# Optimization experiments

Hardware: AMD Instinct MI355X
Metric: run time of the kernel (lower is better)

Reference implementation:

```python
import jax, jax.numpy as jnp
import numpy as np

N = 131072       # active sparse sites (fixed)
C_IN = 256       # FPN input channels
HID = 512        # CONV_HEAD_DIM
K = 9            # 3x3 kernel taps
LAYERS = 8       # NUM_STACKED_CONVS
GROUPS = 32      # GroupNorm groups (detectron2 default)
EPS = 1e-5


def _build_rulebook(rng):
    # Sample sparse occupancy over 64 ROIs of 64x64, build 3x3 neighbor map.
    B, H, W = 64, 64, 64
    mask = rng.random((B, H, W)) < 0.60
    coords = np.argwhere(mask)[:N]          # [N,3] (b,y,x), fixed N
    assert coords.shape[0] == N
    grid = -np.ones((B, H + 2, W + 2), np.int32)  # padded, -1 = inactive
    grid[coords[:, 0], coords[:, 1] + 1, coords[:, 2] + 1] = np.arange(N, dtype=np.int32)
    offs = [(dy, dx) for dy in (-1, 0, 1) for dx in (-1, 0, 1)]
    nbr = np.stack(
        [grid[coords[:, 0], coords[:, 1] + 1 + dy, coords[:, 2] + 1 + dx] for dy, dx in offs],
        axis=1,
    )  # [N,9], -1 where neighbor inactive (submanifold: output sites == input sites)
    return nbr


def setup_inputs() -> dict:
    rng = np.random.default_rng(0)
    nbr = _build_rulebook(rng)
    key = jax.random.key(0)
    k0, k1, k2, k3, k4 = jax.random.split(key, 5)
    features = jax.random.normal(k0, (N, C_IN), jnp.float32)
    w0 = jax.random.normal(k1, (K, C_IN, HID), jnp.float32) * (1.0 / np.sqrt(K * C_IN))
    w_rest = jax.random.normal(k2, (LAYERS - 1, K, HID, HID), jnp.float32) * (1.0 / np.sqrt(K * HID))
    gamma = 1.0 + 0.1 * jax.random.normal(k3, (LAYERS, HID), jnp.float32)
    beta = 0.1 * jax.random.normal(k4, (LAYERS, HID), jnp.float32)
    return {
        "features": features,
        "nbr_idx": jnp.asarray(nbr),
        "w0": w0,
        "w_rest": w_rest,
        "gamma": gamma,
        "beta": beta,
    }


def _subm_conv(x, nbr_idx, w):
    # gather-GEMM-scatter submanifold conv: x [N,Cin], nbr_idx [N,K], w [K,Cin,Cout]
    n = x.shape[0]
    xp = jnp.concatenate([x, jnp.zeros((1, x.shape[1]), x.dtype)], axis=0)  # zero row for -1
    idx = jnp.where(nbr_idx < 0, n, nbr_idx)
    out = jnp.zeros((n, w.shape[2]), x.dtype)
    for k in range(K):  # fixed small loop over kernel taps
        out = out + xp[idx[:, k]] @ w[k]
    return out


def _group_norm(x, g, b):
    # per-point GroupNorm over channel groups: x [N,C]
    n, c = x.shape
    xg = x.reshape(n, GROUPS, c // GROUPS)
    mu = jnp.mean(xg, axis=-1, keepdims=True)
    var = jnp.var(xg, axis=-1, keepdims=True)
    xg = (xg - mu) * jax.lax.rsqrt(var + EPS)
    return xg.reshape(n, c) * g + b


def reference(features, nbr_idx, w0, w_rest, gamma, beta):
    x = jax.nn.relu(_group_norm(_subm_conv(features, nbr_idx, w0), gamma[0], beta[0]))
    for i in range(LAYERS - 1):
        x = jax.nn.relu(_group_norm(_subm_conv(x, nbr_idx, w_rest[i]), gamma[i + 1], beta[i + 1]))
    return x
```

## Files before the change

### kernel.cpp

```cpp
#include <hip/hip_runtime.h>
#include <stdint.h>

#define N_SITES 131072
#define CIN0 256
#define HID 512
#define KTAPS 9
#define NLAYERS 8

typedef __bf16 bf16x8 __attribute__((ext_vector_type(8)));
typedef float f32x4 __attribute__((ext_vector_type(4)));

__device__ __forceinline__ unsigned short f2bf(float f) {
    union { float f; unsigned u; } v; v.f = f;
    return (unsigned short)((v.u + 0x7fffu + ((v.u >> 16) & 1u)) >> 16);
}


__global__ void cvt_features_kernel(const float* __restrict__ in, unsigned short* __restrict__ out) {
    int t = blockIdx.x * 256 + threadIdx.x;
    const float4* p = (const float4*)in + 2 * (size_t)t;
    float4 a = p[0], b = p[1];
    uint4 o;
    o.x = f2bf(a.x) | ((unsigned)f2bf(a.y) << 16);
    o.y = f2bf(a.z) | ((unsigned)f2bf(a.w) << 16);
    o.z = f2bf(b.x) | ((unsigned)f2bf(b.y) << 16);
    o.w = f2bf(b.z) | ((unsigned)f2bf(b.w) << 16);
    ((uint4*)out)[t] = o;
}

__global__ void zero_rows_kernel(unsigned short* __restrict__ xf, unsigned short* __restrict__ xo) {
    int t = threadIdx.x;
    xf[(size_t)N_SITES * 512 + t] = 0;
    xf[(size_t)N_SITES * 512 + 256 + t] = 0;
    xo[(size_t)N_SITES * 256 + t] = 0;
    xo[(size_t)N_SITES * 512 + t] = 0;
    xo[(size_t)N_SITES * 512 + 256 + t] = 0;
}

__global__ void transpose_w_kernel(const float* __restrict__ in, unsigned short* __restrict__ out, int cin) {
    __shared__ float tile[32][33];
    int m = blockIdx.z;
    int nb = blockIdx.x * 32;
    int cb = blockIdx.y * 32;
    int tx = threadIdx.x, ty = threadIdx.y;
    const float* src = in + (size_t)m * cin * HID;
    unsigned short* dst = out + (size_t)m * HID * cin;
#pragma unroll
    for (int j = 0; j < 4; ++j) {
        int r = ty + 8 * j;
        tile[r][tx] = src[(size_t)(cb + r) * HID + nb + tx];
    }
    __syncthreads();
#pragma unroll
    for (int j = 0; j < 4; ++j) {
        int r = ty + 8 * j;
        dst[(size_t)(nb + r) * cin + cb + tx] = f2bf(tile[tx][r]);
    }
}


__device__ __forceinline__ void async16(const void* g, void* l) {
    __builtin_amdgcn_global_load_lds(
        (__attribute__((address_space(1))) unsigned int*)(g),
        (__attribute__((address_space(3))) unsigned int*)(l),
        16, 0, 0);
}

#define BARRIER() do { asm volatile("" ::: "memory"); __builtin_amdgcn_s_barrier(); asm volatile("" ::: "memory"); } while (0)
#define WAIT_LGKM0() asm volatile("s_waitcnt lgkmcnt(0)" ::: "memory")
#define WAIT_VM4() asm volatile("s_waitcnt vmcnt(4)" ::: "memory")
#define WAIT_VM0() asm volatile("s_waitcnt vmcnt(0)" ::: "memory")

#define MFMA4(I, A, B0_, B1_, B2_, B3_) \
    acc[I][0] = __builtin_amdgcn_mfma_f32_16x16x32_bf16(A, B0_, acc[I][0], 0, 0, 0); \
    acc[I][1] = __builtin_amdgcn_mfma_f32_16x16x32_bf16(A, B1_, acc[I][1], 0, 0, 0); \
    acc[I][2] = __builtin_amdgcn_mfma_f32_16x16x32_bf16(A, B2_, acc[I][2], 0, 0, 0); \
    acc[I][3] = __builtin_amdgcn_mfma_f32_16x16x32_bf16(A, B3_, acc[I][3], 0, 0, 0);

template<int CIN>
__global__ __launch_bounds__(512, 2) void subm_gemm_gn_8ph(
    const unsigned short* __restrict__ x,
    const int* __restrict__ nbr,
    const unsigned short* __restrict__ wt,
    const float* __restrict__ gamma,
    const float* __restrict__ beta,
    void* __restrict__ obuf,
    int write_bf16)
{
    constexpr int KK = CIN / 64;
    __shared__ uint4 lds[8192];
    __shared__ int nbrS[256 * KTAPS];

    const int tid = threadIdx.x;
    const int lane = tid & 63;
    const int wave = tid >> 6;
    const int wm = (wave >> 2) * 128;
    const int wn = (wave & 3) * 64;

    const int b = (int)blockIdx.x;
    const int xcd = b & 7;
    const int slot = b >> 3;
    const int colbase = (xcd & 1) * 256;
    const int rowbase = ((xcd >> 1) * 128 + slot) * 256;

    const int srow = 2 * (tid >> 3) + ((tid >> 2) & 1);
    const int scl = (tid & 3) ^ ((tid >> 3) & 3);
    const int ldsw = tid & ~63;

    for (int u = tid; u < 256 * KTAPS; u += 512) {
        int v = nbr[(size_t)rowbase * KTAPS + u];
        nbrS[u] = (v < 0) ? N_SITES : v;
    }
    __syncthreads();

    const f32x4 zero4 = {0.f, 0.f, 0.f, 0.f};
    f32x4 acc[8][4];
#pragma unroll
    for (int i = 0; i < 8; ++i)
#pragma unroll
        for (int j = 0; j < 4; ++j)
            acc[i][j] = zero4;

    auto stageA = [&](int i0, int i1, int kkp, int kh, int buf) {
        const unsigned short* g0 = x + (size_t)i0 * CIN + kkp * 64 + kh * 32 + scl * 8;
        const unsigned short* g1 = x + (size_t)i1 * CIN + kkp * 64 + kh * 32 + scl * 8;
        async16(g0, &lds[buf * 4096 + kh * 1024 + ldsw]);
        async16(g1, &lds[buf * 4096 + kh * 1024 + 512 + ldsw]);
    };
    auto stageB = [&](int tp, int kkp, int kh, int buf) {
        const unsigned short* g0 = wt + (size_t)(tp * HID + colbase + srow) * CIN + kkp * 64 + kh * 32 + scl * 8;
        const unsigned short* g1 = wt + (size_t)(tp * HID + colbase + srow + 128) * CIN + kkp * 64 + kh * 32 + scl * 8;
        async16(g0, &lds[buf * 4096 + 2048 + kh * 1024 + ldsw]);
        async16(g1, &lds[buf * 4096 + 2048 + kh * 1024 + 512 + ldsw]);
    };
    auto rdA = [&](int i, int ks, int buf) {
        int rl = wm + i * 16 + (lane & 15);
        return __builtin_bit_cast(bf16x8,
            lds[buf * 4096 + ks * 1024 + (rl >> 1) * 8 + (rl & 1) * 4 + ((lane >> 4) ^ ((rl >> 1) & 3))]);
    };
    auto rdB = [&](int j, int ks, int buf) {
        int rn = wn + j * 16 + (lane & 15);
        return __builtin_bit_cast(bf16x8,
            lds[buf * 4096 + 2048 + ks * 1024 + (rn >> 1) * 8 + (rn & 1) * 4 + ((lane >> 4) ^ ((rn >> 1) & 3))]);
    };

    {
        int a0 = nbrS[srow * KTAPS], a1 = nbrS[(srow + 128) * KTAPS];
        stageA(a0, a1, 0, 0, 0);
        stageB(0, 0, 0, 0);
        stageA(a0, a1, 0, 1, 0);
        stageB(0, 0, 1, 0);
    }
    WAIT_VM4();
    BARRIER();

    for (int tap = 0; tap < KTAPS; ++tap) {
#pragma unroll 2
        for (int kk = 0; kk < KK; ++kk) {
            const int p = kk & 1;
            const int q = p ^ 1;
            const bool haveNext = !(tap == KTAPS - 1 && kk == KK - 1);
            const int ntap = (kk == KK - 1) ? tap + 1 : tap;
            const int nkk = (kk == KK - 1) ? 0 : kk + 1;
            int nA0 = 0, nA1 = 0;
            if (haveNext) {
                nA0 = nbrS[srow * KTAPS + ntap];
                nA1 = nbrS[(srow + 128) * KTAPS + ntap];
            }
            if (haveNext) stageA(nA0, nA1, nkk, 0, q);
            bf16x8 a0 = rdA(0, 0, p), a1 = rdA(1, 0, p), a2 = rdA(2, 0, p), a3 = rdA(3, 0, p);
            bf16x8 b0 = rdB(0, 0, p), b1 = rdB(1, 0, p), b2 = rdB(2, 0, p), b3 = rdB(3, 0, p);
            BARRIER();
            WAIT_LGKM0();
            __builtin_amdgcn_s_setprio(1);
            MFMA4(0, a0, b0, b1, b2, b3)
            MFMA4(1, a1, b0, b1, b2, b3)
            MFMA4(2, a2, b0, b1, b2, b3)
            MFMA4(3, a3, b0, b1, b2, b3)
            __builtin_amdgcn_s_setprio(0);
            BARRIER();
            if (haveNext) stageB(ntap, nkk, 0, q);
            {
                bf16x8 a4 = rdA(4, 0, p), a5 = rdA(5, 0, p), a6 = rdA(6, 0, p), a7 = rdA(7, 0, p);
                BARRIER();
                WAIT_LGKM0();
                __builtin_amdgcn_s_setprio(1);
                MFMA4(4, a4, b0, b1, b2, b3)
                MFMA4(5, a5, b0, b1, b2, b3)
                MFMA4(6, a6, b0, b1, b2, b3)
                MFMA4(7, a7, b0, b1, b2, b3)
                __builtin_amdgcn_s_setprio(0);
            }
            if (haveNext) { WAIT_VM4(); } else { WAIT_VM0(); }
            BARRIER();
            if (haveNext) stageA(nA0, nA1, nkk, 1, q);
            a0 = rdA(0, 1, p); a1 = rdA(1, 1, p); a2 = rdA(2, 1, p); a3 = rdA(3, 1, p);
            b0 = rdB(0, 1, p); b1 = rdB(1, 1, p); b2 = rdB(2, 1, p); b3 = rdB(3, 1, p);
            BARRIER();
            WAIT_LGKM0();
            __builtin_amdgcn_s_setprio(1);
            MFMA4(0, a0, b0, b1, b2, b3)
            MFMA4(1, a1, b0, b1, b2, b3)
            MFMA4(2, a2, b0, b1, b2, b3)
            MFMA4(3, a3, b0, b1, b2, b3)
            __builtin_amdgcn_s_setprio(0);
            BARRIER();
            if (haveNext) stageB(ntap, nkk, 1, q);
            {
                bf16x8 a4 = rdA(4, 1, p), a5 = rdA(5, 1, p), a6 = rdA(6, 1, p), a7 = rdA(7, 1, p);
                BARRIER();
                WAIT_LGKM0();
                __builtin_amdgcn_s_setprio(1);
                MFMA4(4, a4, b0, b1, b2, b3)
                MFMA4(5, a5, b0, b1, b2, b3)
                MFMA4(6, a6, b0, b1, b2, b3)
                MFMA4(7, a7, b0, b1, b2, b3)
                __builtin_amdgcn_s_setprio(0);
            }
            WAIT_VM4();
            BARRIER();
        }
    }

    __syncthreads();
    float* E = (float*)lds;
    const int seg = tid & 31;
    const int qv = tid >> 5;
    const int c0s = seg * 8;
    unsigned short* bf_out = (unsigned short*)obuf;
    float* f_out = (float*)obuf;

    float gv[8], bv[8];
#pragma unroll
    for (int k = 0; k < 8; ++k) {
        gv[k] = gamma[colbase + c0s + k];
        bv[k] = beta[colbase + c0s + k];
    }

#pragma unroll
    for (int pass = 0; pass < 2; ++pass) {
        if (pass) __syncthreads();
#pragma unroll
        for (int ii = 0; ii < 4; ++ii) {
#pragma unroll
            for (int j = 0; j < 4; ++j) {
                const int col = wn + j * 16 + (lane & 15);
                const int lrow = (wm >> 1) + ii * 16 + (lane >> 4) * 4;
                *(f32x4*)&E[col * 128 + (lrow ^ (((col >> 3) & 7) << 2))] = acc[pass * 4 + ii][j];
            }
        }
        __syncthreads();
#pragma unroll
        for (int h = 0; h < 2; ++h) {
            const int r0w = (qv + h * 16) * 4;
            f32x4 vv[8];
            f32x4 s = zero4, q2 = zero4;
#pragma unroll
            for (int cc = 0; cc < 8; ++cc) {
                const int col = c0s + cc;
                vv[cc] = *(const f32x4*)&E[col * 128 + (r0w ^ (((col >> 3) & 7) << 2))];
                s += vv[cc];
                q2 += vv[cc] * vv[cc];
            }
            f32x4 mu, rs;
#pragma unroll
            for (int r = 0; r < 4; ++r) {
                s[r] += __shfl_xor(s[r], 1);
                q2[r] += __shfl_xor(q2[r], 1);
                mu[r] = s[r] * 0.0625f;
                rs[r] = rsqrtf(q2[r] * 0.0625f - mu[r] * mu[r] + 1e-5f);
            }
            if (write_bf16) {
#pragma unroll
                for (int r = 0; r < 4; ++r) {
                    const int l = r0w + r;
                    const int grow = rowbase + 64 * pass + (l & 63) + ((l >> 6) << 7);
                    unsigned pk[4];
#pragma unroll
                    for (int cp = 0; cp < 4; ++cp) {
                        float ya = fmaxf(0.f, (vv[2 * cp][r] - mu[r]) * rs[r] * gv[2 * cp] + bv[2 * cp]);
                        float yb = fmaxf(0.f, (vv[2 * cp + 1][r] - mu[r]) * rs[r] * gv[2 * cp + 1] + bv[2 * cp + 1]);
                        pk[cp] = f2bf(ya) | ((unsigned)f2bf(yb) << 16);
                    }
                    uint4 o; o.x = pk[0]; o.y = pk[1]; o.z = pk[2]; o.w = pk[3];
                    *(uint4*)&bf_out[(size_t)grow * HID + colbase + c0s] = o;
                }
            } else {
#pragma unroll
                for (int r = 0; r < 4; ++r) {
                    const int l = r0w + r;
                    const int grow = rowbase + 64 * pass + (l & 63) + ((l >> 6) << 7);
                    f32x4 ya, yb;
#pragma unroll
                    for (int k = 0; k < 4; ++k) {
                        ya[k] = fmaxf(0.f, (vv[k][r] - mu[r]) * rs[r] * gv[k] + bv[k]);
                        yb[k] = fmaxf(0.f, (vv[4 + k][r] - mu[r]) * rs[r] * gv[4 + k] + bv[4 + k]);
                    }
                    float* dst = f_out + (size_t)grow * HID + colbase + c0s;
                    *(f32x4*)dst = ya;
                    *(f32x4*)(dst + 4) = yb;
                }
            }
        }
    }
}


extern "C" void kernel_launch(void* const* d_in, const int* in_sizes, int n_in,
                              void* d_out, int out_size, void* d_ws, size_t ws_size,
                              hipStream_t stream) {
    const float* features = (const float*)d_in[0];
    const int*   nbr      = (const int*)d_in[1];
    const float* w0       = (const float*)d_in[2];
    const float* w_rest   = (const float*)d_in[3];
    const float* gamma    = (const float*)d_in[4];
    const float* beta     = (const float*)d_in[5];

    unsigned short* xF = (unsigned short*)d_ws;
    size_t xbytes = (size_t)(N_SITES + 1) * HID * sizeof(unsigned short);
    unsigned short* w0t = (unsigned short*)((char*)d_ws + xbytes);
    size_t w0t_bytes = (size_t)KTAPS * HID * CIN0 * sizeof(unsigned short);
    unsigned short* wrt = (unsigned short*)((char*)d_ws + xbytes + w0t_bytes);
    unsigned short* xO = (unsigned short*)d_out;

    cvt_features_kernel<<<N_SITES * CIN0 / (256 * 8), 256, 0, stream>>>(features, xO);
    zero_rows_kernel<<<1, 256, 0, stream>>>(xF, xO);
    transpose_w_kernel<<<dim3(HID / 32, CIN0 / 32, KTAPS), dim3(32, 8), 0, stream>>>(w0, w0t, CIN0);
    transpose_w_kernel<<<dim3(HID / 32, HID / 32, (NLAYERS - 1) * KTAPS), dim3(32, 8), 0, stream>>>(w_rest, wrt, HID);

    for (int l = 0; l < NLAYERS; ++l) {
        const unsigned short* wt = (l == 0) ? w0t : wrt + (size_t)(l - 1) * KTAPS * HID * HID;
        const unsigned short* xin = (l & 1) ? xF : xO;
        void* obuf = (l == NLAYERS - 1) ? d_out : (void*)((l & 1) ? xO : xF);
        const float* g = gamma + (size_t)l * HID;
        const float* bt = beta + (size_t)l * HID;
        int wb = (l < NLAYERS - 1) ? 1 : 0;
        if (l == 0)
            subm_gemm_gn_8ph<CIN0><<<(N_SITES / 256) * 2, 512, 0, stream>>>(xin, nbr, wt, g, bt, obuf, wb);
        else
            subm_gemm_gn_8ph<HID><<<(N_SITES / 256) * 2, 512, 0, stream>>>(xin, nbr, wt, g, bt, obuf, wb);
    }
}
```

Before: 5.352 ms.

## Shrink block tile to 128 rows with 3-stage single-barrier pipeline

Each block now covers 128 rows instead of 256 (grid doubles), with a 32-wide K step and a three-slot LDS ring buffer. Each iteration issues the loads for two steps ahead and ends with a single barrier, replacing the previous 8-phase schedule that used many barriers per step. LDS use and the accumulator count drop by half, and launch bounds target 4 blocks per CU to raise occupancy. The trade-off is that each weight tile is reused across fewer rows, so weight traffic doubles, and each MFMA burst between barriers is shorter.

```diff
diff --git a/kernel.cpp b/kernel.cpp
--- a/kernel.cpp
+++ b/kernel.cpp
@@ -67,18 +67,11 @@
 }
 
 #define BARRIER() do { asm volatile("" ::: "memory"); __builtin_amdgcn_s_barrier(); asm volatile("" ::: "memory"); } while (0)
-#define WAIT_LGKM0() asm volatile("s_waitcnt lgkmcnt(0)" ::: "memory")
-#define WAIT_VM4() asm volatile("s_waitcnt vmcnt(4)" ::: "memory")
+#define WAIT_VM3() asm volatile("s_waitcnt vmcnt(3)" ::: "memory")
 #define WAIT_VM0() asm volatile("s_waitcnt vmcnt(0)" ::: "memory")
 
-#define MFMA4(I, A, B0_, B1_, B2_, B3_) \
-    acc[I][0] = __builtin_amdgcn_mfma_f32_16x16x32_bf16(A, B0_, acc[I][0], 0, 0, 0); \
-    acc[I][1] = __builtin_amdgcn_mfma_f32_16x16x32_bf16(A, B1_, acc[I][1], 0, 0, 0); \
-    acc[I][2] = __builtin_amdgcn_mfma_f32_16x16x32_bf16(A, B2_, acc[I][2], 0, 0, 0); \
-    acc[I][3] = __builtin_amdgcn_mfma_f32_16x16x32_bf16(A, B3_, acc[I][3], 0, 0, 0);
-
 template<int CIN>
-__global__ __launch_bounds__(512, 2) void subm_gemm_gn_8ph(
+__global__ __launch_bounds__(512, 4) void subm_gemm_gn_p2(
     const unsigned short* __restrict__ x,
     const int* __restrict__ nbr,
     const unsigned short* __restrict__ wt,
@@ -87,139 +80,94 @@
     void* __restrict__ obuf,
     int write_bf16)
 {
-    constexpr int KK = CIN / 64;
-    __shared__ uint4 lds[8192];
-    __shared__ int nbrS[256 * KTAPS];
+    constexpr int KK = CIN / 32;
+    __shared__ uint4 lds[4608];
+    __shared__ int nbrS[128 * KTAPS];
 
     const int tid = threadIdx.x;
     const int lane = tid & 63;
     const int wave = tid >> 6;
-    const int wm = (wave >> 2) * 128;
+    const int wm = (wave >> 2) * 64;
     const int wn = (wave & 3) * 64;
 
     const int b = (int)blockIdx.x;
     const int xcd = b & 7;
     const int slot = b >> 3;
     const int colbase = (xcd & 1) * 256;
-    const int rowbase = ((xcd >> 1) * 128 + slot) * 256;
+    const int rowbase = ((xcd >> 1) * 256 + slot) * 128;
 
     const int srow = 2 * (tid >> 3) + ((tid >> 2) & 1);
     const int scl = (tid & 3) ^ ((tid >> 3) & 3);
     const int ldsw = tid & ~63;
 
-    for (int u = tid; u < 256 * KTAPS; u += 512) {
+    for (int u = tid; u < 128 * KTAPS; u += 512) {
         int v = nbr[(size_t)rowbase * KTAPS + u];
         nbrS[u] = (v < 0) ? N_SITES : v;
     }
     __syncthreads();
 
     const f32x4 zero4 = {0.f, 0.f, 0.f, 0.f};
-    f32x4 acc[8][4];
-#pragma unroll
-    for (int i = 0; i < 8; ++i)
+    f32x4 acc[4][4];
+#pragma unroll
+    for (int i = 0; i < 4; ++i)
 #pragma unroll
         for (int j = 0; j < 4; ++j)
             acc[i][j] = zero4;
 
-    auto stageA = [&](int i0, int i1, int kkp, int kh, int buf) {
-        const unsigned short* g0 = x + (size_t)i0 * CIN + kkp * 64 + kh * 32 + scl * 8;
-        const unsigned short* g1 = x + (size_t)i1 * CIN + kkp * 64 + kh * 32 + scl * 8;
-        async16(g0, &lds[buf * 4096 + kh * 1024 + ldsw]);
-        async16(g1, &lds[buf * 4096 + kh * 1024 + 512 + ldsw]);
-    };
-    auto stageB = [&](int tp, int kkp, int kh, int buf) {
-        const unsigned short* g0 = wt + (size_t)(tp * HID + colbase + srow) * CIN + kkp * 64 + kh * 32 + scl * 8;
-        const unsigned short* g1 = wt + (size_t)(tp * HID + colbase + srow + 128) * CIN + kkp * 64 + kh * 32 + scl * 8;
-        async16(g0, &lds[buf * 4096 + 2048 + kh * 1024 + ldsw]);
-        async16(g1, &lds[buf * 4096 + 2048 + kh * 1024 + 512 + ldsw]);
-    };
-    auto rdA = [&](int i, int ks, int buf) {
+    auto stageA = [&](int trow, int kk2, int s) {
+        async16(x + (size_t)trow * CIN + kk2 * 32 + scl * 8, &lds[s * 512 + ldsw]);
+    };
+    auto stageB = [&](int ttap, int kk2, int s) {
+        const unsigned short* g = wt + ((size_t)ttap * HID + colbase + srow) * CIN + kk2 * 32 + scl * 8;
+        async16(g, &lds[1536 + s * 1024 + ldsw]);
+        async16(g + (size_t)128 * CIN, &lds[1536 + s * 1024 + 512 + ldsw]);
+    };
+    auto rdA = [&](int i, int s) {
         int rl = wm + i * 16 + (lane & 15);
         return __builtin_bit_cast(bf16x8,
-            lds[buf * 4096 + ks * 1024 + (rl >> 1) * 8 + (rl & 1) * 4 + ((lane >> 4) ^ ((rl >> 1) & 3))]);
-    };
-    auto rdB = [&](int j, int ks, int buf) {
+            lds[s * 512 + (rl >> 1) * 8 + (rl & 1) * 4 + ((lane >> 4) ^ ((rl >> 1) & 3))]);
+    };
+    auto rdB = [&](int j, int s) {
         int rn = wn + j * 16 + (lane & 15);
         return __builtin_bit_cast(bf16x8,
-            lds[buf * 4096 + 2048 + ks * 1024 + (rn >> 1) * 8 + (rn & 1) * 4 + ((lane >> 4) ^ ((rn >> 1) & 3))]);
-    };
-
-    {
-        int a0 = nbrS[srow * KTAPS], a1 = nbrS[(srow + 128) * KTAPS];
-        stageA(a0, a1, 0, 0, 0);
-        stageB(0, 0, 0, 0);
-        stageA(a0, a1, 0, 1, 0);
-        stageB(0, 0, 1, 0);
-    }
-    WAIT_VM4();
+            lds[1536 + s * 1024 + (rn >> 1) * 8 + (rn & 1) * 4 + ((lane >> 4) ^ ((rn >> 1) & 3))]);
+    };
+
+    int rcur = nbrS[srow * KTAPS + 0];
+    stageA(rcur, 0, 0);
+    stageB(0, 0, 0);
+    stageA(rcur, 1, 1);
+    stageB(0, 1, 1);
+    WAIT_VM3();
     BARRIER();
 
+    int cur = 0;
     for (int tap = 0; tap < KTAPS; ++tap) {
-#pragma unroll 2
+        const int rnext = (tap + 1 < KTAPS) ? nbrS[srow * KTAPS + tap + 1] : 0;
         for (int kk = 0; kk < KK; ++kk) {
-            const int p = kk & 1;
-            const int q = p ^ 1;
-            const bool haveNext = !(tap == KTAPS - 1 && kk == KK - 1);
-            const int ntap = (kk == KK - 1) ? tap + 1 : tap;
-            const int nkk = (kk == KK - 1) ? 0 : kk + 1;
-            int nA0 = 0, nA1 = 0;
-            if (haveNext) {
-                nA0 = nbrS[srow * KTAPS + ntap];
-                nA1 = nbrS[(srow + 128) * KTAPS + ntap];
-            }
-            if (haveNext) stageA(nA0, nA1, nkk, 0, q);
-            bf16x8 a0 = rdA(0, 0, p), a1 = rdA(1, 0, p), a2 = rdA(2, 0, p), a3 = rdA(3, 0, p);
-            bf16x8 b0 = rdB(0, 0, p), b1 = rdB(1, 0, p), b2 = rdB(2, 0, p), b3 = rdB(3, 0, p);
+            const bool haveStage = !(tap == KTAPS - 1 && kk >= KK - 2);
+            const int stg = (cur >= 1) ? cur - 1 : 2;
+            if (haveStage) {
+                int kk2 = kk + 2, ttap = tap, trow = rcur;
+                if (kk2 >= KK) { kk2 -= KK; ttap = tap + 1; trow = rnext; }
+                stageA(trow, kk2, stg);
+                stageB(ttap, kk2, stg);
+            }
+            bf16x8 af[4], bfr[4];
+#pragma unroll
+            for (int f = 0; f < 4; ++f) { af[f] = rdA(f, cur); bfr[f] = rdB(f, cur); }
+            __builtin_amdgcn_s_setprio(1);
+#pragma unroll
+            for (int i = 0; i < 4; ++i)
+#pragma unroll
+                for (int j = 0; j < 4; ++j)
+                    acc[i][j] = __builtin_amdgcn_mfma_f32_16x16x32_bf16(af[i], bfr[j], acc[i][j], 0, 0, 0);
+            __builtin_amdgcn_s_setprio(0);
+            if (haveStage) { WAIT_VM3(); } else { WAIT_VM0(); }
             BARRIER();
-            WAIT_LGKM0();
-            __builtin_amdgcn_s_setprio(1);
-            MFMA4(0, a0, b0, b1, b2, b3)
-            MFMA4(1, a1, b0, b1, b2, b3)
-            MFMA4(2, a2, b0, b1, b2, b3)
-            MFMA4(3, a3, b0, b1, b2, b3)
-            __builtin_amdgcn_s_setprio(0);
-            BARRIER();
-            if (haveNext) stageB(ntap, nkk, 0, q);
-            {
-                bf16x8 a4 = rdA(4, 0, p), a5 = rdA(5, 0, p), a6 = rdA(6, 0, p), a7 = rdA(7, 0, p);
-                BARRIER();
-                WAIT_LGKM0();
-                __builtin_amdgcn_s_setprio(1);
-                MFMA4(4, a4, b0, b1, b2, b3)
-                MFMA4(5, a5, b0, b1, b2, b3)
-                MFMA4(6, a6, b0, b1, b2, b3)
-                MFMA4(7, a7, b0, b1, b2, b3)
-                __builtin_amdgcn_s_setprio(0);
-            }
-            if (haveNext) { WAIT_VM4(); } else { WAIT_VM0(); }
-            BARRIER();
-            if (haveNext) stageA(nA0, nA1, nkk, 1, q);
-            a0 = rdA(0, 1, p); a1 = rdA(1, 1, p); a2 = rdA(2, 1, p); a3 = rdA(3, 1, p);
-            b0 = rdB(0, 1, p); b1 = rdB(1, 1, p); b2 = rdB(2, 1, p); b3 = rdB(3, 1, p);
-            BARRIER();
-            WAIT_LGKM0();
-            __builtin_amdgcn_s_setprio(1);
-            MFMA4(0, a0, b0, b1, b2, b3)
-            MFMA4(1, a1, b0, b1, b2, b3)
-            MFMA4(2, a2, b0, b1, b2, b3)
-            MFMA4(3, a3, b0, b1, b2, b3)
-            __builtin_amdgcn_s_setprio(0);
-            BARRIER();
-            if (haveNext) stageB(ntap, nkk, 1, q);
-            {
-                bf16x8 a4 = rdA(4, 1, p), a5 = rdA(5, 1, p), a6 = rdA(6, 1, p), a7 = rdA(7, 1, p);
-                BARRIER();
-                WAIT_LGKM0();
-                __builtin_amdgcn_s_setprio(1);
-                MFMA4(4, a4, b0, b1, b2, b3)
-                MFMA4(5, a5, b0, b1, b2, b3)
-                MFMA4(6, a6, b0, b1, b2, b3)
-                MFMA4(7, a7, b0, b1, b2, b3)
-                __builtin_amdgcn_s_setprio(0);
-            }
-            WAIT_VM4();
-            BARRIER();
-        }
+            cur = (cur < 2) ? cur + 1 : 0;
+        }
+        rcur = rnext;
     }
 
     __syncthreads();
@@ -236,70 +184,67 @@
         gv[k] = gamma[colbase + c0s + k];
         bv[k] = beta[colbase + c0s + k];
     }
+    const int growbase = rowbase + (qv >> 3) * 64 + ((qv >> 2) & 1) * 16 + (qv & 3) * 4;
 
 #pragma unroll
     for (int pass = 0; pass < 2; ++pass) {
         if (pass) __syncthreads();
 #pragma unroll
-        for (int ii = 0; ii < 4; ++ii) {
+        for (int ii = 0; ii < 2; ++ii) {
 #pragma unroll
             for (int j = 0; j < 4; ++j) {
                 const int col = wn + j * 16 + (lane & 15);
                 const int lrow = (wm >> 1) + ii * 16 + (lane >> 4) * 4;
-                *(f32x4*)&E[col * 128 + (lrow ^ (((col >> 3) & 7) << 2))] = acc[pass * 4 + ii][j];
+                *(f32x4*)&E[col * 64 + (lrow ^ (((col >> 3) & 7) << 2))] = acc[pass * 2 + ii][j];
             }
         }
         __syncthreads();
-#pragma unroll
-        for (int h = 0; h < 2; ++h) {
-            const int r0w = (qv + h * 16) * 4;
-            f32x4 vv[8];
-            f32x4 s = zero4, q2 = zero4;
-#pragma unroll
-            for (int cc = 0; cc < 8; ++cc) {
-                const int col = c0s + cc;
-                vv[cc] = *(const f32x4*)&E[col * 128 + (r0w ^ (((col >> 3) & 7) << 2))];
-                s += vv[cc];
-                q2 += vv[cc] * vv[cc];
-            }
-            f32x4 mu, rs;
+
+        const int r0w = qv * 4;
+        f32x4 vv[8];
+        f32x4 s = zero4, q2 = zero4;
+#pragma unroll
+        for (int cc = 0; cc < 8; ++cc) {
+            const int col = c0s + cc;
+            vv[cc] = *(const f32x4*)&E[col * 64 + (r0w ^ (((col >> 3) & 7) << 2))];
+            s += vv[cc];
+            q2 += vv[cc] * vv[cc];
+        }
+        f32x4 mu, rs;
+#pragma unroll
+        for (int r = 0; r < 4; ++r) {
+            s[r] += __shfl_xor(s[r], 1);
+            q2[r] += __shfl_xor(q2[r], 1);
+            mu[r] = s[r] * 0.0625f;
+            rs[r] = rsqrtf(q2[r] * 0.0625f - mu[r] * mu[r] + 1e-5f);
+        }
+        if (write_bf16) {
 #pragma unroll
             for (int r = 0; r < 4; ++r) {
-                s[r] += __shfl_xor(s[r], 1);
-                q2[r] += __shfl_xor(q2[r], 1);
-                mu[r] = s[r] * 0.0625f;
-                rs[r] = rsqrtf(q2[r] * 0.0625f - mu[r] * mu[r] + 1e-5f);
-            }
-            if (write_bf16) {
-#pragma unroll
-                for (int r = 0; r < 4; ++r) {
-                    const int l = r0w + r;
-                    const int grow = rowbase + 64 * pass + (l & 63) + ((l >> 6) << 7);
-                    unsigned pk[4];
-#pragma unroll
-                    for (int cp = 0; cp < 4; ++cp) {
-                        float ya = fmaxf(0.f, (vv[2 * cp][r] - mu[r]) * rs[r] * gv[2 * cp] + bv[2 * cp]);
-                        float yb = fmaxf(0.f, (vv[2 * cp + 1][r] - mu[r]) * rs[r] * gv[2 * cp + 1] + bv[2 * cp + 1]);
-                        pk[cp] = f2bf(ya) | ((unsigned)f2bf(yb) << 16);
-                    }
-                    uint4 o; o.x = pk[0]; o.y = pk[1]; o.z = pk[2]; o.w = pk[3];
-                    *(uint4*)&bf_out[(size_t)grow * HID + colbase + c0s] = o;
+                const int grow = growbase + pass * 32 + r;
+                unsigned pk[4];
+#pragma unroll
+                for (int cp = 0; cp < 4; ++cp) {
+                    float ya = fmaxf(0.f, (vv[2 * cp][r] - mu[r]) * rs[r] * gv[2 * cp] + bv[2 * cp]);
+                    float yb = fmaxf(0.f, (vv[2 * cp + 1][r] - mu[r]) * rs[r] * gv[2 * cp + 1] + bv[2 * cp + 1]);
+                    pk[cp] = f2bf(ya) | ((unsigned)f2bf(yb) << 16);
                 }
-            } else {
-#pragma unroll
-                for (int r = 0; r < 4; ++r) {
-                    const int l = r0w + r;
-                    const int grow = rowbase + 64 * pass + (l & 63) + ((l >> 6) << 7);
-                    f32x4 ya, yb;
-#pragma unroll
-                    for (int k = 0; k < 4; ++k) {
-                        ya[k] = fmaxf(0.f, (vv[k][r] - mu[r]) * rs[r] * gv[k] + bv[k]);
-                        yb[k] = fmaxf(0.f, (vv[4 + k][r] - mu[r]) * rs[r] * gv[4 + k] + bv[4 + k]);
-                    }
-                    float* dst = f_out + (size_t)grow * HID + colbase + c0s;
-                    *(f32x4*)dst = ya;
-                    *(f32x4*)(dst + 4) = yb;
+                uint4 o; o.x = pk[0]; o.y = pk[1]; o.z = pk[2]; o.w = pk[3];
+                *(uint4*)&bf_out[(size_t)grow * HID + colbase + c0s] = o;
+            }
+        } else {
+#pragma unroll
+            for (int r = 0; r < 4; ++r) {
+                const int grow = growbase + pass * 32 + r;
+                f32x4 ya, yb;
+#pragma unroll
+                for (int k = 0; k < 4; ++k) {
+                    ya[k] = fmaxf(0.f, (vv[k][r] - mu[r]) * rs[r] * gv[k] + bv[k]);
+                    yb[k] = fmaxf(0.f, (vv[4 + k][r] - mu[r]) * rs[r] * gv[4 + k] + bv[4 + k]);
                 }
+                float* dst = f_out + (size_t)grow * HID + colbase + c0s;
+                *(f32x4*)dst = ya;
+                *(f32x4*)(dst + 4) = yb;
             }
         }
     }
@@ -336,8 +281,8 @@
         const float* bt = beta + (size_t)l * HID;
         int wb = (l < NLAYERS - 1) ? 1 : 0;
         if (l == 0)
-            subm_gemm_gn_8ph<CIN0><<<(N_SITES / 256) * 2, 512, 0, stream>>>(xin, nbr, wt, g, bt, obuf, wb);
+            subm_gemm_gn_p2<CIN0><<<(N_SITES / 128) * 2, 512, 0, stream>>>(xin, nbr, wt, g, bt, obuf, wb);
         else
-            subm_gemm_gn_8ph<HID><<<(N_SITES / 256) * 2, 512, 0, stream>>>(xin, nbr, wt, g, bt, obuf, wb);
-    }
-}
+            subm_gemm_gn_p2<HID><<<(N_SITES / 128) * 2, 512, 0, stream>>>(xin, nbr, wt, g, bt, obuf, wb);
+    }
+}
```

Result: faster. 4.868 ms (-9.0%).
